# Kernel optimization log

Hardware: AMD Instinct MI355X
Metric: run time of the kernel (lower is better)

The kernel has to match this reference:

```python
import jax, jax.numpy as jnp
import numpy as np

S, H, A = 16384, 1024, 1024


def setup_inputs() -> dict:
    key = jax.random.key(0)
    k1, k2, k3, k4, k5, k6 = jax.random.split(key, 6)
    enc_out = jax.random.normal(k1, (S, 1, H), dtype=jnp.float32)
    dec_h = jax.random.normal(k2, (1, H), dtype=jnp.float32)
    mask = jax.random.randint(k3, (S, 1), 0, 2) == 1  # bool [S,1]
    # learned params (torch Linear stores weight as [out, in]; y = x @ W.T)
    W2_dec = jax.random.normal(k4, (A, H), dtype=jnp.float32) * 0.02
    W1_enc = jax.random.normal(k5, (A, H), dtype=jnp.float32) * 0.02
    V = jax.random.normal(k6, (1, A), dtype=jnp.float32) * 0.02
    return {"enc_out": enc_out, "dec_h": dec_h, "mask": mask,
            "W2_dec": W2_dec, "W1_enc": W1_enc, "V": V}


def reference(enc_out, dec_h, mask, W2_dec, W1_enc, V):
    enc = jnp.squeeze(enc_out, axis=1)            # [S, H]
    d = dec_h @ W2_dec.T                          # [1, A]
    e = enc @ W1_enc.T                            # [S, A]
    u = jnp.tanh(d + e) @ V.T                     # [S, 1]
    u = jnp.where(mask, -jnp.inf, u)              # masked logits (returned, like in-place fill)
    a = jax.nn.softmax(u, axis=0)                 # softmax over seq dim
    out = jnp.sum(a * enc, axis=0)                # [H]
    return (out, u)
```

## Files before the change

### kernel.cpp

```cpp
#include <hip/hip_runtime.h>
#include <math.h>
#include <stdint.h>

#define S_DIM 16384
#define H_DIM 1024
#define A_DIM 1024

#define MASK_NEG (-3.0e38f)

typedef __attribute__((ext_vector_type(8))) _Float16 f16x8;
typedef __attribute__((ext_vector_type(4))) float f32x4;
typedef __attribute__((address_space(3))) uint32_t as3_u32;
typedef __attribute__((address_space(1))) uint32_t as1_u32;

__global__ __launch_bounds__(256) void prep_kernel(
        const float* __restrict__ enc, _Float16* __restrict__ enc_h,
        const float* __restrict__ W1, _Float16* __restrict__ W1_h,
        const float* __restrict__ dec_h, const float* __restrict__ W2,
        float* __restrict__ d, float* __restrict__ u_acc) {
    const int b = blockIdx.x;
    const int t = threadIdx.x;
    if (b < 8704) {
        const float* src = (b < 8192) ? enc : W1;
        _Float16* dst    = (b < 8192) ? enc_h : W1_h;
        const int i = ((b < 8192) ? b : (b - 8192)) * 256 + t;
        float4 v0 = ((const float4*)src)[2 * i];
        float4 v1 = ((const float4*)src)[2 * i + 1];
        union { _Float16 h[8]; uint4 u; } pk;
        pk.h[0] = (_Float16)v0.x; pk.h[1] = (_Float16)v0.y;
        pk.h[2] = (_Float16)v0.z; pk.h[3] = (_Float16)v0.w;
        pk.h[4] = (_Float16)v1.x; pk.h[5] = (_Float16)v1.y;
        pk.h[6] = (_Float16)v1.z; pk.h[7] = (_Float16)v1.w;
        ((uint4*)dst)[i] = pk.u;
        if (b < 64) u_acc[b * 256 + t] = 0.0f;
    } else {
        const int a = b - 8704;
        const float* row = W2 + (size_t)a * H_DIM;
        float s = 0.0f;
        for (int h = t; h < H_DIM; h += 256) s += dec_h[h] * row[h];
        #pragma unroll
        for (int off = 32; off; off >>= 1) s += __shfl_down(s, off, 64);
        __shared__ float wsum[4];
        if ((t & 63) == 0) wsum[t >> 6] = s;
        __syncthreads();
        if (t == 0) d[a] = wsum[0] + wsum[1] + wsum[2] + wsum[3];
    }
}

__global__ __launch_bounds__(256) void fused_gemm_f16(
        const _Float16* __restrict__ Ag,
        const _Float16* __restrict__ Bg,
        const float* __restrict__ V,
        const float* __restrict__ d,
        float* __restrict__ u_acc) {
    __shared__ _Float16 At[2][128 * 32];
    __shared__ _Float16 Bt[2][128 * 32];
    __shared__ float P[128][2];

    const int tid  = threadIdx.x;
    const int wave = tid >> 6;
    const int lane = tid & 63;
    const int quad = lane >> 4;
    const int l16  = lane & 15;
    const int wm   = wave >> 1;
    const int wn   = wave & 1;
    const int s0   = blockIdx.x * 128;
    const int a0   = blockIdx.y * 128;

    const _Float16* gsrc = (wave < 2) ? Ag : Bg;
    _Float16* tbase      = (wave < 2) ? &At[0][0] : &Bt[0][0];
    const int rbase      = (wave < 2) ? s0 : a0;
    const int rowoff     = (wave & 1) * 64;
    const int lrow = lane >> 2;
    const int cg   = ((lane & 3) + (lrow >> 1)) & 3;

    const _Float16* grow[4];
    #pragma unroll
    for (int j = 0; j < 4; ++j)
        grow[j] = gsrc + (size_t)(rbase + rowoff + j * 16 + lrow) * H_DIM + cg * 8;
    _Float16* lrow0 = tbase + rowoff * 32;

    const int sw = ((quad - (l16 >> 1)) & 3) * 8;
    int aoff[4], boff[4];
    #pragma unroll
    for (int f = 0; f < 4; ++f) {
        aoff[f] = (wm * 64 + f * 16 + l16) * 32 + sw;
        boff[f] = (wn * 64 + f * 16 + l16) * 32 + sw;
    }

    f32x4 acc[4][4];
    #pragma unroll
    for (int mi = 0; mi < 4; ++mi)
        #pragma unroll
        for (int ni = 0; ni < 4; ++ni)
            acc[mi][ni] = (f32x4){0.f, 0.f, 0.f, 0.f};

    {
        #pragma unroll
        for (int j = 0; j < 4; ++j)
            __builtin_amdgcn_global_load_lds(
                (const as1_u32*)(const void*)(grow[j]),
                (as3_u32*)(void*)(lrow0 + j * 512), 16, 0, 0);
    }
    __syncthreads();

    for (int kt = 0; kt < H_DIM / 32; kt += 2) {
        {
            #pragma unroll
            for (int j = 0; j < 4; ++j)
                __builtin_amdgcn_global_load_lds(
                    (const as1_u32*)(const void*)(grow[j] + (kt + 1) * 32),
                    (as3_u32*)(void*)(lrow0 + 4096 + j * 512), 16, 0, 0);
        }
        {
            f16x8 bf[4];
            #pragma unroll
            for (int ni = 0; ni < 4; ++ni) bf[ni] = *(const f16x8*)&Bt[0][boff[ni]];
            #pragma unroll
            for (int mi = 0; mi < 4; ++mi) {
                f16x8 af = *(const f16x8*)&At[0][aoff[mi]];
                #pragma unroll
                for (int ni = 0; ni < 4; ++ni)
                    acc[mi][ni] = __builtin_amdgcn_mfma_f32_16x16x32_f16(af, bf[ni], acc[mi][ni], 0, 0, 0);
            }
        }
        __syncthreads();

        if (kt + 2 < H_DIM / 32) {
            #pragma unroll
            for (int j = 0; j < 4; ++j)
                __builtin_amdgcn_global_load_lds(
                    (const as1_u32*)(const void*)(grow[j] + (kt + 2) * 32),
                    (as3_u32*)(void*)(lrow0 + j * 512), 16, 0, 0);
        }
        {
            f16x8 bf[4];
            #pragma unroll
            for (int ni = 0; ni < 4; ++ni) bf[ni] = *(const f16x8*)&Bt[1][boff[ni]];
            #pragma unroll
            for (int mi = 0; mi < 4; ++mi) {
                f16x8 af = *(const f16x8*)&At[1][aoff[mi]];
                #pragma unroll
                for (int ni = 0; ni < 4; ++ni)
                    acc[mi][ni] = __builtin_amdgcn_mfma_f32_16x16x32_f16(af, bf[ni], acc[mi][ni], 0, 0, 0);
            }
        }
        __syncthreads();
    }

    float vv[4], dd[4];
    #pragma unroll
    for (int ni = 0; ni < 4; ++ni) {
        int c = a0 + wn * 64 + ni * 16 + l16;
        vv[ni] = V[c];
        dd[ni] = d[c];
    }
    #pragma unroll
    for (int mi = 0; mi < 4; ++mi) {
        #pragma unroll
        for (int reg = 0; reg < 4; ++reg) {
            float s = 0.0f;
            #pragma unroll
            for (int ni = 0; ni < 4; ++ni)
                s += vv[ni] * tanhf(dd[ni] + acc[mi][ni][reg]);
            #pragma unroll
            for (int off = 1; off < 16; off <<= 1)
                s += __shfl_xor(s, off, 64);
            if (l16 == 0)
                P[wm * 64 + mi * 16 + quad * 4 + reg][wn] = s;
        }
    }
    __syncthreads();
    if (tid < 128)
        atomicAdd(u_acc + s0 + tid, P[tid][0] + P[tid][1]);
}

__global__ __launch_bounds__(256) void fused_gemm(const float* __restrict__ enc,
                                                  const float* __restrict__ W1,
                                                  const float* __restrict__ V,
                                                  const float* __restrict__ d,
                                                  float* __restrict__ u_acc) {
    __shared__ __align__(16) float As[16][128 + 4];
    __shared__ __align__(16) float Bs[16][128 + 4];
    const int tid = threadIdx.x;
    const int tx = tid & 15, ty = tid >> 4;
    const int s0 = blockIdx.y * 128, a0 = blockIdx.x * 128;
    const int lr = tid >> 2, lc = tid & 3;
    float acc[8][8] = {};
    for (int kt = 0; kt < H_DIM / 16; ++kt) {
        const int k0 = kt * 16;
        float4 av0 = *(const float4*)(enc + (size_t)(s0 + lr)      * H_DIM + k0 + 4 * lc);
        float4 av1 = *(const float4*)(enc + (size_t)(s0 + lr + 64) * H_DIM + k0 + 4 * lc);
        float4 bv0 = *(const float4*)(W1  + (size_t)(a0 + lr)      * H_DIM + k0 + 4 * lc);
        float4 bv1 = *(const float4*)(W1  + (size_t)(a0 + lr + 64) * H_DIM + k0 + 4 * lc);
        __syncthreads();
        As[4*lc+0][lr] = av0.x; As[4*lc+1][lr] = av0.y; As[4*lc+2][lr] = av0.z; As[4*lc+3][lr] = av0.w;
        As[4*lc+0][lr+64] = av1.x; As[4*lc+1][lr+64] = av1.y; As[4*lc+2][lr+64] = av1.z; As[4*lc+3][lr+64] = av1.w;
        Bs[4*lc+0][lr] = bv0.x; Bs[4*lc+1][lr] = bv0.y; Bs[4*lc+2][lr] = bv0.z; Bs[4*lc+3][lr] = bv0.w;
        Bs[4*lc+0][lr+64] = bv1.x; Bs[4*lc+1][lr+64] = bv1.y; Bs[4*lc+2][lr+64] = bv1.z; Bs[4*lc+3][lr+64] = bv1.w;
        __syncthreads();
        #pragma unroll
        for (int k = 0; k < 16; ++k) {
            float4 A0 = *(const float4*)&As[k][8 * ty];
            float4 A1 = *(const float4*)&As[k][8 * ty + 4];
            float4 B0 = *(const float4*)&Bs[k][8 * tx];
            float4 B1 = *(const float4*)&Bs[k][8 * tx + 4];
            float ar[8] = {A0.x, A0.y, A0.z, A0.w, A1.x, A1.y, A1.z, A1.w};
            float br[8] = {B0.x, B0.y, B0.z, B0.w, B1.x, B1.y, B1.z, B1.w};
            #pragma unroll
            for (int i = 0; i < 8; ++i)
                #pragma unroll
                for (int j = 0; j < 8; ++j)
                    acc[i][j] = fmaf(ar[i], br[j], acc[i][j]);
        }
    }
    float vv[8], dd[8];
    #pragma unroll
    for (int j = 0; j < 8; ++j) { int c = a0 + 8 * tx + j; vv[j] = V[c]; dd[j] = d[c]; }
    float pu[8];
    #pragma unroll
    for (int i = 0; i < 8; ++i) {
        float s = 0.0f;
        #pragma unroll
        for (int j = 0; j < 8; ++j) s += vv[j] * tanhf(dd[j] + acc[i][j]);
        pu[i] = s;
    }
    __syncthreads();
    float* Pf = &As[0][0];
    #pragma unroll
    for (int i = 0; i < 8; ++i) Pf[(8 * ty + i) * 16 + tx] = pu[i];
    __syncthreads();
    if (tid < 128) {
        float s = 0.0f;
        #pragma unroll
        for (int j = 0; j < 16; ++j) s += Pf[tid * 16 + j];
        atomicAdd(u_acc + s0 + tid, s);
    }
}

__global__ __launch_bounds__(1024) void softmax_kernel(const float* __restrict__ u_acc,
                                                       const void* __restrict__ mask,
                                                       float* __restrict__ u_out,
                                                       float* __restrict__ p) {
    const int t = threadIdx.x;
    const unsigned char* mb = (const unsigned char*)mask;
    const int* mi = (const int*)mask;

    unsigned int orv = 0;
    for (int i = t; i < S_DIM; i += 1024)
        if (i & 3) orv |= mb[i];
    __shared__ int sflag;
    if (t == 0) sflag = 0;
    __syncthreads();
    if (orv) sflag = 1;
    __syncthreads();
    const int bytemask = sflag;

    float v[16];
    float lmax = -INFINITY;
    #pragma unroll
    for (int i = 0; i < 16; ++i) {
        int r = t + i * 1024;
        int m = bytemask ? (int)mb[r] : mi[r];
        float val = m ? MASK_NEG : u_acc[r];
        u_out[r] = val;
        v[i] = val;
        lmax = fmaxf(lmax, val);
    }

    __shared__ float red[16];
    __shared__ float sm, sdenom;
    #pragma unroll
    for (int off = 32; off; off >>= 1) lmax = fmaxf(lmax, __shfl_down(lmax, off, 64));
    int wid = t >> 6, lane = t & 63;
    if (lane == 0) red[wid] = lmax;
    __syncthreads();
    if (t == 0) {
        float m2 = -INFINITY;
        for (int i = 0; i < 16; ++i) m2 = fmaxf(m2, red[i]);
        sm = m2;
    }
    __syncthreads();
    const float m = sm;

    float lsum = 0.0f;
    #pragma unroll
    for (int i = 0; i < 16; ++i) {
        v[i] = expf(v[i] - m);
        lsum += v[i];
    }
    #pragma unroll
    for (int off = 32; off; off >>= 1) lsum += __shfl_down(lsum, off, 64);
    if (lane == 0) red[wid] = lsum;
    __syncthreads();
    if (t == 0) {
        float s2 = 0.0f;
        for (int i = 0; i < 16; ++i) s2 += red[i];
        sdenom = s2;
    }
    __syncthreads();
    const float inv = 1.0f / sdenom;
    #pragma unroll
    for (int i = 0; i < 16; ++i) p[t + i * 1024] = v[i] * inv;
}

__global__ __launch_bounds__(256) void wsum_part(const _Float16* __restrict__ enc_h,
                                                 const float* __restrict__ p,
                                                 float* __restrict__ part) {
    const int t = threadIdx.x;
    const int b = blockIdx.x;
    float4 acc = {0.f, 0.f, 0.f, 0.f};
    const int s0 = b * 32;
    for (int s = s0; s < s0 + 32; ++s) {
        float ps = p[s];
        union { _Float16 h[4]; uint2 u; } e;
        e.u = ((const uint2*)(enc_h + (size_t)s * H_DIM))[t];
        acc.x += ps * (float)e.h[0];
        acc.y += ps * (float)e.h[1];
        acc.z += ps * (float)e.h[2];
        acc.w += ps * (float)e.h[3];
    }
    ((float4*)(part + (size_t)b * 1024))[t] = acc;
}
__global__ __launch_bounds__(256) void wsum_reduce(const float* __restrict__ part,
                                                   float* __restrict__ out) {
    __shared__ float red[256];
    const int t = threadIdx.x;
    const int col = blockIdx.x * 16 + (t & 15);
    const int seg = t >> 4;
    float s = 0.0f;
    for (int b = seg * 32; b < seg * 32 + 32; ++b)
        s += part[(size_t)b * 1024 + col];
    red[t] = s;
    __syncthreads();
    if (t < 16) {
        float r = 0.0f;
        #pragma unroll
        for (int k = 0; k < 16; ++k) r += red[k * 16 + t];
        out[col] = r;
    }
}
__global__ __launch_bounds__(256) void weighted_sum(const float* __restrict__ enc,
                                                    const float* __restrict__ p,
                                                    float* __restrict__ out) {
    const int t = threadIdx.x;
    const int s0 = blockIdx.x * 32;
    const float4* encv = (const float4*)enc;
    float4 acc = {0.0f, 0.0f, 0.0f, 0.0f};
    for (int s = s0; s < s0 + 32; ++s) {
        float ps = p[s];
        float4 e = encv[(size_t)s * 256 + t];
        acc.x += ps * e.x; acc.y += ps * e.y; acc.z += ps * e.z; acc.w += ps * e.w;
    }
    atomicAdd(out + 4 * t + 0, acc.x);
    atomicAdd(out + 4 * t + 1, acc.y);
    atomicAdd(out + 4 * t + 2, acc.z);
    atomicAdd(out + 4 * t + 3, acc.w);
}
__global__ void zero_kernel(float* __restrict__ u_acc, float* __restrict__ out) {
    int i = blockIdx.x * 256 + threadIdx.x;
    if (i < S_DIM) u_acc[i] = 0.0f;
    if (i < H_DIM) out[i]   = 0.0f;
}
__global__ __launch_bounds__(256) void dec_proj(const float* __restrict__ dec_h,
                                                const float* __restrict__ W2,
                                                float* __restrict__ d) {
    int a = blockIdx.x;
    int t = threadIdx.x;
    const float* row = W2 + (size_t)a * H_DIM;
    float s = 0.0f;
    for (int h = t; h < H_DIM; h += 256) s += dec_h[h] * row[h];
    #pragma unroll
    for (int off = 32; off; off >>= 1) s += __shfl_down(s, off, 64);
    __shared__ float wsum[4];
    if ((t & 63) == 0) wsum[t >> 6] = s;
    __syncthreads();
    if (t == 0) d[a] = wsum[0] + wsum[1] + wsum[2] + wsum[3];
}

extern "C" void kernel_launch(void* const* d_in, const int* in_sizes, int n_in,
                              void* d_out, int out_size, void* d_ws, size_t ws_size,
                              hipStream_t stream) {
    const float* enc   = (const float*)d_in[0];
    const float* dec_h = (const float*)d_in[1];
    const void*  mask  = d_in[2];
    const float* W2    = (const float*)d_in[3];
    const float* W1    = (const float*)d_in[4];
    const float* V     = (const float*)d_in[5];

    float* out   = (float*)d_out;
    float* u_out = (float*)d_out + H_DIM;

    float* ws    = (float*)d_ws;
    float* d     = ws;
    float* u_acc = ws + A_DIM;
    float* p     = ws + A_DIM + S_DIM;
    float* part  = ws + A_DIM + 2 * S_DIM;
    size_t f_end = (size_t)(A_DIM + 2 * S_DIM + 512 * 1024);
    _Float16* enc_h = (_Float16*)(ws + f_end);
    _Float16* W1_h  = enc_h + (size_t)S_DIM * H_DIM;
    size_t need_bytes = f_end * 4
                      + (size_t)S_DIM * H_DIM * 2
                      + (size_t)A_DIM * H_DIM * 2;

    if (ws_size >= need_bytes) {
        prep_kernel<<<9728, 256, 0, stream>>>(enc, enc_h, W1, W1_h,
                                              dec_h, W2, d, u_acc);
        fused_gemm_f16<<<dim3(S_DIM / 128, A_DIM / 128), 256, 0, stream>>>(
            enc_h, W1_h, V, d, u_acc);
        softmax_kernel<<<1, 1024, 0, stream>>>(u_acc, mask, u_out, p);
        wsum_part<<<S_DIM / 32, 256, 0, stream>>>(enc_h, p, part);
        wsum_reduce<<<64, 256, 0, stream>>>(part, out);
    } else {
        zero_kernel<<<64, 256, 0, stream>>>(u_acc, out);
        dec_proj<<<A_DIM, 256, 0, stream>>>(dec_h, W2, d);
        fused_gemm<<<dim3(A_DIM / 128, S_DIM / 128), 256, 0, stream>>>(enc, W1, V, d, u_acc);
        softmax_kernel<<<1, 1024, 0, stream>>>(u_acc, mask, u_out, p);
        weighted_sum<<<S_DIM / 32, 256, 0, stream>>>(enc, p, out);
    }
}
```

Before: 203.7 us.

## Enlarge f16 MFMA GEMM tile to 256x256 with 512-thread blocks

The fused fp16 GEMM+tanh+V-projection kernel now uses 256x256 output tiles per block with 8 waves (2x4 layout), each wave computing 128x64 instead of 64x64. This raises arithmetic intensity per LDS load and halves global/LDS traffic per FLOP, and also halves the number of atomicAdds into u_acc per row. It costs a 64 KB shared buffer that is reused for the partial-sum reduction, higher register pressure (32 accumulator fragments), and fewer blocks (256 total), which may hurt occupancy and the tail across the CUs.

```diff
diff --git a/kernel.cpp b/kernel.cpp
--- a/kernel.cpp
+++ b/kernel.cpp
@@ -47,30 +47,27 @@
     }
 }
 
-__global__ __launch_bounds__(256) void fused_gemm_f16(
+__global__ __launch_bounds__(512, 2) void fused_gemm_f16(
         const _Float16* __restrict__ Ag,
         const _Float16* __restrict__ Bg,
         const float* __restrict__ V,
         const float* __restrict__ d,
         float* __restrict__ u_acc) {
-    __shared__ _Float16 At[2][128 * 32];
-    __shared__ _Float16 Bt[2][128 * 32];
-    __shared__ float P[128][2];
+    __shared__ __align__(16) _Float16 AB[2][16384];
 
     const int tid  = threadIdx.x;
     const int wave = tid >> 6;
     const int lane = tid & 63;
     const int quad = lane >> 4;
     const int l16  = lane & 15;
-    const int wm   = wave >> 1;
-    const int wn   = wave & 1;
-    const int s0   = blockIdx.x * 128;
-    const int a0   = blockIdx.y * 128;
-
-    const _Float16* gsrc = (wave < 2) ? Ag : Bg;
-    _Float16* tbase      = (wave < 2) ? &At[0][0] : &Bt[0][0];
-    const int rbase      = (wave < 2) ? s0 : a0;
-    const int rowoff     = (wave & 1) * 64;
+    const int wm   = wave >> 2;
+    const int wn   = wave & 3;
+    const int s0   = blockIdx.x * 256;
+    const int a0   = blockIdx.y * 256;
+
+    const _Float16* gsrc = (wave < 4) ? Ag : Bg;
+    const int rbase      = (wave < 4) ? s0 : a0;
+    const int rowoff     = (wave & 3) * 64;
     const int lrow = lane >> 2;
     const int cg   = ((lane & 3) + (lrow >> 1)) & 3;
 
@@ -78,30 +75,29 @@
     #pragma unroll
     for (int j = 0; j < 4; ++j)
         grow[j] = gsrc + (size_t)(rbase + rowoff + j * 16 + lrow) * H_DIM + cg * 8;
-    _Float16* lrow0 = tbase + rowoff * 32;
+    _Float16* lbase0 = &AB[0][((wave < 4) ? 0 : 8192) + rowoff * 32];
 
     const int sw = ((quad - (l16 >> 1)) & 3) * 8;
-    int aoff[4], boff[4];
-    #pragma unroll
-    for (int f = 0; f < 4; ++f) {
-        aoff[f] = (wm * 64 + f * 16 + l16) * 32 + sw;
-        boff[f] = (wn * 64 + f * 16 + l16) * 32 + sw;
-    }
-
-    f32x4 acc[4][4];
-    #pragma unroll
-    for (int mi = 0; mi < 4; ++mi)
+    int aoff[8], boff[4];
+    #pragma unroll
+    for (int mi = 0; mi < 8; ++mi)
+        aoff[mi] = (wm * 128 + mi * 16 + l16) * 32 + sw;
+    #pragma unroll
+    for (int ni = 0; ni < 4; ++ni)
+        boff[ni] = 8192 + (wn * 64 + ni * 16 + l16) * 32 + sw;
+
+    f32x4 acc[8][4];
+    #pragma unroll
+    for (int mi = 0; mi < 8; ++mi)
         #pragma unroll
         for (int ni = 0; ni < 4; ++ni)
             acc[mi][ni] = (f32x4){0.f, 0.f, 0.f, 0.f};
 
-    {
-        #pragma unroll
-        for (int j = 0; j < 4; ++j)
-            __builtin_amdgcn_global_load_lds(
-                (const as1_u32*)(const void*)(grow[j]),
-                (as3_u32*)(void*)(lrow0 + j * 512), 16, 0, 0);
-    }
+    #pragma unroll
+    for (int j = 0; j < 4; ++j)
+        __builtin_amdgcn_global_load_lds(
+            (const as1_u32*)(const void*)(grow[j]),
+            (as3_u32*)(void*)(lbase0 + j * 512), 16, 0, 0);
     __syncthreads();
 
     for (int kt = 0; kt < H_DIM / 32; kt += 2) {
@@ -110,15 +106,15 @@
             for (int j = 0; j < 4; ++j)
                 __builtin_amdgcn_global_load_lds(
                     (const as1_u32*)(const void*)(grow[j] + (kt + 1) * 32),
-                    (as3_u32*)(void*)(lrow0 + 4096 + j * 512), 16, 0, 0);
+                    (as3_u32*)(void*)(lbase0 + 16384 + j * 512), 16, 0, 0);
         }
         {
             f16x8 bf[4];
             #pragma unroll
-            for (int ni = 0; ni < 4; ++ni) bf[ni] = *(const f16x8*)&Bt[0][boff[ni]];
-            #pragma unroll
-            for (int mi = 0; mi < 4; ++mi) {
-                f16x8 af = *(const f16x8*)&At[0][aoff[mi]];
+            for (int ni = 0; ni < 4; ++ni) bf[ni] = *(const f16x8*)&AB[0][boff[ni]];
+            #pragma unroll
+            for (int mi = 0; mi < 8; ++mi) {
+                f16x8 af = *(const f16x8*)&AB[0][aoff[mi]];
                 #pragma unroll
                 for (int ni = 0; ni < 4; ++ni)
                     acc[mi][ni] = __builtin_amdgcn_mfma_f32_16x16x32_f16(af, bf[ni], acc[mi][ni], 0, 0, 0);
@@ -131,15 +127,15 @@
             for (int j = 0; j < 4; ++j)
                 __builtin_amdgcn_global_load_lds(
                     (const as1_u32*)(const void*)(grow[j] + (kt + 2) * 32),
-                    (as3_u32*)(void*)(lrow0 + j * 512), 16, 0, 0);
+                    (as3_u32*)(void*)(lbase0 + j * 512), 16, 0, 0);
         }
         {
             f16x8 bf[4];
             #pragma unroll
-            for (int ni = 0; ni < 4; ++ni) bf[ni] = *(const f16x8*)&Bt[1][boff[ni]];
-            #pragma unroll
-            for (int mi = 0; mi < 4; ++mi) {
-                f16x8 af = *(const f16x8*)&At[1][aoff[mi]];
+            for (int ni = 0; ni < 4; ++ni) bf[ni] = *(const f16x8*)&AB[1][boff[ni]];
+            #pragma unroll
+            for (int mi = 0; mi < 8; ++mi) {
+                f16x8 af = *(const f16x8*)&AB[1][aoff[mi]];
                 #pragma unroll
                 for (int ni = 0; ni < 4; ++ni)
                     acc[mi][ni] = __builtin_amdgcn_mfma_f32_16x16x32_f16(af, bf[ni], acc[mi][ni], 0, 0, 0);
@@ -148,6 +144,7 @@
         __syncthreads();
     }
 
+    float* P = (float*)&AB[0][0];
     float vv[4], dd[4];
     #pragma unroll
     for (int ni = 0; ni < 4; ++ni) {
@@ -156,7 +153,7 @@
         dd[ni] = d[c];
     }
     #pragma unroll
-    for (int mi = 0; mi < 4; ++mi) {
+    for (int mi = 0; mi < 8; ++mi) {
         #pragma unroll
         for (int reg = 0; reg < 4; ++reg) {
             float s = 0.0f;
@@ -167,12 +164,13 @@
             for (int off = 1; off < 16; off <<= 1)
                 s += __shfl_xor(s, off, 64);
             if (l16 == 0)
-                P[wm * 64 + mi * 16 + quad * 4 + reg][wn] = s;
-        }
-    }
-    __syncthreads();
-    if (tid < 128)
-        atomicAdd(u_acc + s0 + tid, P[tid][0] + P[tid][1]);
+                P[(wm * 128 + mi * 16 + quad * 4 + reg) * 4 + wn] = s;
+        }
+    }
+    __syncthreads();
+    if (tid < 256)
+        atomicAdd(u_acc + s0 + tid,
+                  P[tid * 4 + 0] + P[tid * 4 + 1] + P[tid * 4 + 2] + P[tid * 4 + 3]);
 }
 
 __global__ __launch_bounds__(256) void fused_gemm(const float* __restrict__ enc,
@@ -406,7 +404,7 @@
     if (ws_size >= need_bytes) {
         prep_kernel<<<9728, 256, 0, stream>>>(enc, enc_h, W1, W1_h,
                                               dec_h, W2, d, u_acc);
-        fused_gemm_f16<<<dim3(S_DIM / 128, A_DIM / 128), 256, 0, stream>>>(
+        fused_gemm_f16<<<dim3(S_DIM / 256, A_DIM / 256), 512, 0, stream>>>(
             enc_h, W1_h, V, d, u_acc);
         softmax_kernel<<<1, 1024, 0, stream>>>(u_acc, mask, u_out, p);
         wsum_part<<<S_DIM / 32, 256, 0, stream>>>(enc_h, p, part);
```

Result: faster. 187.9 us (-7.7%).
